# Performance work log

Hardware: AMD Instinct MI355X
Metric: run time of the kernel (lower is better)

The kernel has to match this reference:

```python
import jax, jax.numpy as jnp
import numpy as np
import math

B, S, E, H, L = 16, 512, 256, 4, 2
D = E // H            # head size = 64
MAX_POS = 10
NUM_ITEMS = 50000


def setup_inputs() -> dict:
    key = jax.random.key(0)
    ks = jax.random.split(key, 16)
    s = 0.02
    item_inputs = jax.random.randint(ks[0], (B, S), 0, 2 * NUM_ITEMS + 1)
    item_ids = jax.random.randint(ks[1], (B, S), 0, NUM_ITEMS)
    input_embed = jax.random.normal(ks[2], (2 * NUM_ITEMS + 1, E), jnp.float32) * s
    input_embed = input_embed.at[0].set(0.0)  # padding_idx=0
    query_embed = jax.random.normal(ks[3], (NUM_ITEMS, E), jnp.float32) * s
    pos_key = jax.random.normal(ks[4], (MAX_POS, D), jnp.float32) * s
    pos_value = jax.random.normal(ks[5], (MAX_POS, D), jnp.float32) * s
    Wq = jax.random.normal(ks[6], (L, E, E), jnp.float32) * s
    bq = jnp.zeros((L, E), jnp.float32)
    Wk = jax.random.normal(ks[7], (L, E, E), jnp.float32) * s
    bk = jnp.zeros((L, E), jnp.float32)
    Wv = jax.random.normal(ks[8], (L, E, E), jnp.float32) * s
    bv = jnp.zeros((L, E), jnp.float32)
    Wo = jax.random.normal(ks[9], (L, E, E), jnp.float32) * s
    bo = jnp.zeros((L, E), jnp.float32)
    out_w = jax.random.normal(ks[10], (E, 1), jnp.float32) * s
    out_b = jnp.zeros((1,), jnp.float32)
    return dict(item_inputs=item_inputs, item_ids=item_ids,
                input_embed=input_embed, query_embed=query_embed,
                pos_key=pos_key, pos_value=pos_value,
                Wq=Wq, bq=bq, Wk=Wk, bk=bk, Wv=Wv, bv=bv, Wo=Wo, bo=bo,
                out_w=out_w, out_b=out_b)


def _heads(x, W, b):
    # [B,S,E] @ [E,E] -> [B,H,S,D]
    return (x @ W + b).reshape(B, S, H, D).transpose(0, 2, 1, 3)


def reference(item_inputs, item_ids, input_embed, query_embed, pos_key,
              pos_value, Wq, bq, Wk, bk, Wv, bv, Wo, bo, out_w, out_b):
    x = input_embed[item_inputs]          # [B,S,E]
    q_base = query_embed[item_ids]        # [B,S,E]

    i = jnp.arange(S)
    rel = jnp.clip(i[:, None] - i[None, :], 0, MAX_POS - 1)  # [S,S]
    pk = pos_key[rel]                     # [S,S,D]
    pv = pos_value[rel]                   # [S,S,D]
    causal = i[None, :] > i[:, None]      # future mask [S,S], True = masked
    scale = 1.0 / math.sqrt(D)

    out = x
    for l in range(L):
        qh = _heads(q_base, Wq[l], bq[l])
        kh = _heads(out, Wk[l], bk[l])
        vh = _heads(out, Wv[l], bv[l])
        # relative attention: scores = q.k^T + q.pos_key(i-j)
        scores = jnp.einsum('bhid,bhjd->bhij', qh, kh)
        scores = scores + jnp.einsum('bhid,ijd->bhij', qh, pk)
        scores = scores * scale
        scores = jnp.where(causal[None, None], -1e9, scores)
        p = jax.nn.softmax(scores, axis=-1)  # [B,H,S,S]
        # out_i = sum_j p_ij * (v_j + pos_value(i-j))
        attn = jnp.einsum('bhij,bhjd->bhid', p, vh) \
             + jnp.einsum('bhij,ijd->bhid', p, pv)
        merged = attn.transpose(0, 2, 1, 3).reshape(B, S, E)
        residual = merged @ Wo[l] + bo[l]
        out = out + jax.nn.relu(residual)
    return out @ out_w + out_b            # [B,S,1]
```

## Files before the change

kernel.cpp:

```cpp
#include <hip/hip_runtime.h>
#include <hip/hip_bf16.h>

#define B_ 16
#define S_ 512
#define E_ 256
#define H_ 4
#define D_ 64
#define L_ 2
#define MAXPOS 10
#define HS_ ((size_t)B_ * S_ * E_)

typedef __attribute__((ext_vector_type(8))) short bf16x8;
typedef __attribute__((ext_vector_type(4))) float f32x4;

static __device__ __forceinline__ short f2bf(float f) {
    __hip_bfloat16 h = __float2bfloat16(f);
    return __builtin_bit_cast(short, h);
}

static __device__ __forceinline__ void gload16(const void* g, void* l) {
    __builtin_amdgcn_global_load_lds(
        (const __attribute__((address_space(1))) void*)(g),
        (__attribute__((address_space(3))) void*)(l),
        16, 0, 0);
}

static __device__ __forceinline__ void stage_tile(const char* gbase, char* lds,
                                                  int w, int lane) {
    #pragma unroll
    for (int c = 0; c < 8; ++c) {
        const int L = (w * 8 + c) * 1024 + lane * 16;
        const int src = L ^ (((L >> 9) & 7) << 4);
        gload16(gbase + src, lds + (w * 8 + c) * 1024);
    }
}

static __device__ __forceinline__ void gemm4(const short* As, const short* Bs,
                                             int w, int l15, int l4,
                                             f32x4& a0, f32x4& a1,
                                             f32x4& a2, f32x4& a3) {
    const int sw = (l15 & 7) << 4;
    const int arow = w * 16 + l15;
    const f32x4 z4 = (f32x4){0.f, 0.f, 0.f, 0.f};
    a0 = z4; a1 = z4; a2 = z4; a3 = z4;
    #pragma unroll
    for (int ks = 0; ks < 8; ++ks) {
        const int coff = (ks * 64 + l4 * 16) ^ sw;
        const bf16x8 af = *reinterpret_cast<const bf16x8*>((const char*)As + arow * 512 + coff);
        const bf16x8 b0 = *reinterpret_cast<const bf16x8*>((const char*)Bs + (0 * 16 + l15) * 512 + coff);
        a0 = __builtin_amdgcn_mfma_f32_16x16x32_bf16(af, b0, a0, 0, 0, 0);
        const bf16x8 b1 = *reinterpret_cast<const bf16x8*>((const char*)Bs + (1 * 16 + l15) * 512 + coff);
        a1 = __builtin_amdgcn_mfma_f32_16x16x32_bf16(af, b1, a1, 0, 0, 0);
        const bf16x8 b2 = *reinterpret_cast<const bf16x8*>((const char*)Bs + (2 * 16 + l15) * 512 + coff);
        a2 = __builtin_amdgcn_mfma_f32_16x16x32_bf16(af, b2, a2, 0, 0, 0);
        const bf16x8 b3 = *reinterpret_cast<const bf16x8*>((const char*)Bs + (3 * 16 + l15) * 512 + coff);
        a3 = __builtin_amdgcn_mfma_f32_16x16x32_bf16(af, b3, a3, 0, 0, 0);
    }
}

static __device__ __forceinline__ void gemm_compute(const short* As, const short* Bs,
                                                    f32x4* acc, int w, int l15, int l4) {
    gemm4(As, Bs, w, l15, l4, acc[0], acc[1], acc[2], acc[3]);
}

__global__ __launch_bounds__(256) void setup_kernel(
    const int* __restrict__ item_inputs, const int* __restrict__ item_ids,
    const float* __restrict__ input_embed, const float* __restrict__ query_embed,
    const float* __restrict__ Wq, const float* __restrict__ Wk,
    const float* __restrict__ Wv, const float* __restrict__ Wo,
    const float* __restrict__ out_b,
    float* __restrict__ outf, short* __restrict__ outb, short* __restrict__ qbb,
    short* __restrict__ Wt, float* __restrict__ y)
{
    const int tid = threadIdx.x;
    const int bx = blockIdx.x;
    if (bx < 512) {
        const int rr = tid >> 4, c0 = (tid & 15) * 16;
        const int row = bx * 16 + rr;
        const int ii = item_inputs[row];
        const int qi = item_ids[row];
        const float* xs = input_embed + (size_t)ii * E_ + c0;
        const float* qs = query_embed + (size_t)qi * E_ + c0;
        float* of = outf + (size_t)row * E_ + c0;
        short* ob = outb + (size_t)row * E_ + c0;
        short* qb = qbb + (size_t)row * E_ + c0;
        #pragma unroll
        for (int q = 0; q < 4; ++q) {
            const float4 xv = reinterpret_cast<const float4*>(xs)[q];
            const float4 qv = reinterpret_cast<const float4*>(qs)[q];
            reinterpret_cast<float4*>(of)[q] = xv;
            short4 xb = { f2bf(xv.x), f2bf(xv.y), f2bf(xv.z), f2bf(xv.w) };
            short4 qb4 = { f2bf(qv.x), f2bf(qv.y), f2bf(qv.z), f2bf(qv.w) };
            reinterpret_cast<short4*>(ob)[q] = xb;
            reinterpret_cast<short4*>(qb)[q] = qb4;
        }
        return;
    }
    const int pb = bx - 512;
    if (pb < 128) {
        __shared__ short tt[64 * 72];
        const int mId = pb >> 4;
        const int l = mId >> 2, which = mId & 3;
        const float* src = (which == 0 ? Wq : which == 1 ? Wk : which == 2 ? Wv : Wo)
                         + (size_t)l * E_ * E_;
        const int tr = (pb >> 2) & 3;
        const int tc = pb & 3;
        {
            const int kl = tid >> 2;
            const int nq = (tid & 3) * 16;
            const float* sp = src + (size_t)(tr * 64 + kl) * E_ + tc * 64 + nq;
            #pragma unroll
            for (int q = 0; q < 4; ++q) {
                const float4 v = reinterpret_cast<const float4*>(sp)[q];
                tt[(nq + q * 4 + 0) * 72 + kl] = f2bf(v.x);
                tt[(nq + q * 4 + 1) * 72 + kl] = f2bf(v.y);
                tt[(nq + q * 4 + 2) * 72 + kl] = f2bf(v.z);
                tt[(nq + q * 4 + 3) * 72 + kl] = f2bf(v.w);
            }
        }
        __syncthreads();
        {
            const int nl = tid >> 2;
            const int kq = (tid & 3) * 16;
            short* dst = Wt + (size_t)mId * 65536 + (size_t)(tc * 64 + nl) * E_ + tr * 64 + kq;
            *reinterpret_cast<bf16x8*>(&dst[0]) = *reinterpret_cast<const bf16x8*>(&tt[nl * 72 + kq]);
            *reinterpret_cast<bf16x8*>(&dst[8]) = *reinterpret_cast<const bf16x8*>(&tt[nl * 72 + kq + 8]);
        }
    } else if (pb == 128) {
        const float yb = out_b[0];
        for (int i = tid; i < 8192; i += 256) y[i] = yb;
    }
}

__global__ __launch_bounds__(256) void qkv_kernel(
    const short* __restrict__ qbb, const short* __restrict__ outb,
    const short* __restrict__ Wt, const float* __restrict__ bq,
    const float* __restrict__ bk, const float* __restrict__ bv,
    short* __restrict__ Qb)
{
    __shared__ __align__(16) short As[64 * 256];
    __shared__ __align__(16) short Bs[64 * 256];
    const int bm = blockIdx.x, bn = blockIdx.y, z = blockIdx.z;
    const int tid = threadIdx.x;
    const int lane = tid & 63, w = tid >> 6;
    const int l15 = lane & 15, l4 = lane >> 4;

    const short* A = (z == 0) ? qbb : outb;
    const short* W = Wt + (size_t)z * 65536;
    const float* bias = (z == 0) ? bq : (z == 1) ? bk : bv;

    stage_tile((const char*)A + (size_t)bm * 32768, (char*)As, w, lane);
    stage_tile((const char*)W + (size_t)bn * 32768, (char*)Bs, w, lane);
    __syncthreads();

    f32x4 acc[4];
    gemm_compute(As, Bs, acc, w, l15, l4);

    short* Cz = Qb + (size_t)z * HS_;
    #pragma unroll
    for (int nf = 0; nf < 4; ++nf) {
        const int col = bn * 64 + nf * 16 + l15;
        const float bb = bias[col];
        #pragma unroll
        for (int reg = 0; reg < 4; ++reg) {
            const int rowg = bm * 64 + w * 16 + l4 * 4 + reg;
            Cz[(size_t)rowg * E_ + col] = f2bf(acc[nf][reg] + bb);
        }
    }
}

__global__ __launch_bounds__(256) void o0_kernel(
    const short* __restrict__ mgb, const short* __restrict__ Wo_t,
    const float* __restrict__ bo0, float* __restrict__ outf,
    short* __restrict__ outb)
{
    __shared__ __align__(16) short As[64 * 256];
    __shared__ __align__(16) short Bs[64 * 256];
    const int bm = blockIdx.x, bn = blockIdx.y;
    const int tid = threadIdx.x;
    const int lane = tid & 63, w = tid >> 6;
    const int l15 = lane & 15, l4 = lane >> 4;

    stage_tile((const char*)mgb + (size_t)bm * 32768, (char*)As, w, lane);
    stage_tile((const char*)Wo_t + (size_t)bn * 32768, (char*)Bs, w, lane);
    __syncthreads();

    f32x4 acc[4];
    gemm_compute(As, Bs, acc, w, l15, l4);

    #pragma unroll
    for (int nf = 0; nf < 4; ++nf) {
        const int col = bn * 64 + nf * 16 + l15;
        const float bb = bo0[col];
        #pragma unroll
        for (int reg = 0; reg < 4; ++reg) {
            const int rowg = bm * 64 + w * 16 + l4 * 4 + reg;
            const size_t idx = (size_t)rowg * E_ + col;
            const float o = outf[idx] + fmaxf(acc[nf][reg] + bb, 0.0f);
            outf[idx] = o;
            outb[idx] = f2bf(o);
        }
    }
}

__global__ __launch_bounds__(256) void attn2_kernel(
    const short* __restrict__ Q, const short* __restrict__ K,
    const short* __restrict__ V, const float* __restrict__ pos_key,
    const float* __restrict__ pos_value, short* __restrict__ merged)
{
    __shared__ __align__(16) short Qs[64 * 72];
    __shared__ __align__(16) short Ks[64 * 64];
    __shared__ __align__(16) short Vts[4656];
    __shared__ __align__(16) short Pl[4 * 16 * 72];
    __shared__ __align__(16) short Pk[16 * 72];
    __shared__ float pv_sh[MAXPOS * 64];
    __shared__ float qpk_sh[64 * 16];
    __shared__ float pdiag[64 * 9];

    const int bid = blockIdx.x;
    const int a = bid & 3;
    const int h = (bid >> 2) & 3;
    const int b = bid >> 4;
    const int tid = threadIdx.x;
    const int lane = tid & 63;
    const int w = tid >> 6;
    const int l15 = lane & 15;
    const int l4  = lane >> 4;
    const int rloc  = l4 * 4;
    const int rbase = w * 16 + rloc;
    const int swl = (l15 & 7) << 4;

    const size_t boff = (size_t)(b * S_) * E_ + h * D_;

    for (int idx = tid; idx < MAXPOS * 64; idx += 256) pv_sh[idx] = pos_value[idx];
    for (int idx = tid; idx < 16 * 64; idx += 256) {
        const int r = idx >> 6, d = idx & 63;
        Pk[r * 72 + d] = (r < MAXPOS) ? f2bf(pos_key[r * 64 + d]) : (short)0;
    }

    for (int pass = 0; pass < 2; ++pass) {
        const int it = pass ? a : 7 - a;
        if (pass) __syncthreads();
        for (int idx = tid; idx < 64 * 9; idx += 256) pdiag[idx] = 0.0f;
        {
            const int row = tid >> 2, dq = (tid & 3) * 16;
            const short* qp = &Q[boff + (size_t)(it * 64 + row) * E_ + dq];
            *reinterpret_cast<bf16x8*>(&Qs[row * 72 + dq]) = *reinterpret_cast<const bf16x8*>(qp);
            *reinterpret_cast<bf16x8*>(&Qs[row * 72 + dq + 8]) = *reinterpret_cast<const bf16x8*>(qp + 8);
        }
        __syncthreads();

        bf16x8 aq[2];
        #pragma unroll
        for (int ks = 0; ks < 2; ++ks)
            aq[ks] = *reinterpret_cast<const bf16x8*>(&Qs[(w * 16 + l15) * 72 + ks * 32 + 8 * l4]);

        f32x4 cq = (f32x4){0.f, 0.f, 0.f, 0.f};
        #pragma unroll
        for (int ks = 0; ks < 2; ++ks) {
            const bf16x8 bpk = *reinterpret_cast<const bf16x8*>(&Pk[l15 * 72 + ks * 32 + 8 * l4]);
            cq = __builtin_amdgcn_mfma_f32_16x16x32_bf16(aq[ks], bpk, cq, 0, 0, 0);
        }
        float q9[4];
        #pragma unroll
        for (int r = 0; r < 4; ++r) {
            qpk_sh[(rbase + r) * 16 + l15] = cq[r] * 0.125f;
            q9[r] = __shfl(cq[r], l4 * 16 + 9, 64) * 0.125f;
        }

        f32x4 accv[4];
        #pragma unroll
        for (int nf = 0; nf < 4; ++nf) accv[nf] = (f32x4){0.f, 0.f, 0.f, 0.f};
        float ls[4] = {0.f, 0.f, 0.f, 0.f};

        for (int jt = 0; jt <= it; ++jt) {
            {
                const char* Kb = (const char*)(K + boff + (size_t)(jt * 64) * E_);
                #pragma unroll
                for (int c = 0; c < 2; ++c) {
                    const int chunk = w * 2 + c;
                    const int row = chunk * 8 + (lane >> 3);
                    const int col = (lane & 7) * 16;
                    const int src = row * 512 + (col ^ ((row & 7) << 4));
                    gload16(Kb + src, (char*)Ks + chunk * 1024);
                }
                const int row = tid >> 2, dq = (tid & 3) * 16;
                const short* vp = &V[boff + (size_t)(jt * 64 + row) * E_ + dq];
                const bf16x8 v0 = *reinterpret_cast<const bf16x8*>(vp);
                const bf16x8 v1 = *reinterpret_cast<const bf16x8*>(vp + 8);
                const int skew = (tid & 3) * 32 + row * 2;
                #pragma unroll
                for (int e = 0; e < 8; ++e) {
                    *(short*)((char*)Vts + (dq + e) * 144 + skew) = v0[e];
                    *(short*)((char*)Vts + (dq + 8 + e) * 144 + skew) = v1[e];
                }
            }
            __syncthreads();

            const bool near = (jt >= it - 1);
            #pragma unroll
            for (int nf = 0; nf < 4; ++nf) {
                f32x4 c = (f32x4){0.f, 0.f, 0.f, 0.f};
                const int jrow = nf * 16 + l15;
                const bf16x8 bk0 = *reinterpret_cast<const bf16x8*>(
                    (const char*)Ks + jrow * 128 + ((l4 * 16) ^ swl));
                const bf16x8 bk1 = *reinterpret_cast<const bf16x8*>(
                    (const char*)Ks + jrow * 128 + ((64 + l4 * 16) ^ swl));
                c = __builtin_amdgcn_mfma_f32_16x16x32_bf16(aq[0], bk0, c, 0, 0, 0);
                c = __builtin_amdgcn_mfma_f32_16x16x32_bf16(aq[1], bk1, c, 0, 0, 0);
                const int j = jt * 64 + nf * 16 + l15;
                #pragma unroll
                for (int r = 0; r < 4; ++r) {
                    float pp;
                    if (near) {
                        const int i = it * 64 + rbase + r;
                        const int rel = i - j;
                        if (rel < 0) pp = 0.0f;
                        else {
                            const int rc = rel < 9 ? rel : 9;
                            pp = __expf(fmaf(c[r], 0.125f, qpk_sh[(rbase + r) * 16 + rc]));
                            if (rel < 9) pdiag[(rbase + r) * 9 + rel] = pp;
                        }
                    } else {
                        pp = __expf(fmaf(c[r], 0.125f, q9[r]));
                    }
                    ls[r] += pp;
                    Pl[w * 1152 + (rloc + r) * 72 + nf * 16 + l15] = f2bf(pp);
                }
            }
            #pragma unroll
            for (int ks = 0; ks < 2; ++ks) {
                const bf16x8 pa = *reinterpret_cast<const bf16x8*>(
                    &Pl[w * 1152 + l15 * 72 + ks * 32 + 8 * l4]);
                #pragma unroll
                for (int nf = 0; nf < 4; ++nf) {
                    const int d = nf * 16 + l15;
                    const bf16x8 bv = *reinterpret_cast<const bf16x8*>(
                        (const char*)Vts + d * 144 + nf * 32 + ks * 64 + l4 * 16);
                    accv[nf] = __builtin_amdgcn_mfma_f32_16x16x32_bf16(pa, bv, accv[nf], 0, 0, 0);
                }
            }
            __syncthreads();
        }

        #pragma unroll
        for (int m = 1; m < 16; m <<= 1) {
            #pragma unroll
            for (int r = 0; r < 4; ++r) ls[r] += __shfl_xor(ls[r], m, 64);
        }

        #pragma unroll
        for (int r = 0; r < 4; ++r) {
            const int rowl = rbase + r;
            const float inv = 1.0f / ls[r];
            #pragma unroll
            for (int nf = 0; nf < 4; ++nf) {
                const int col = nf * 16 + l15;
                const float pv9 = pv_sh[9 * 64 + col];
                float extra = ls[r] * pv9;
                #pragma unroll
                for (int rr = 0; rr < 9; ++rr)
                    extra += pdiag[rowl * 9 + rr] * (pv_sh[rr * 64 + col] - pv9);
                merged[boff + (size_t)(it * 64 + rowl) * E_ + col] =
                    f2bf((accv[nf][r] + extra) * inv);
            }
        }
    }
}

__global__ __launch_bounds__(256) void o1final_kernel(
    const short* __restrict__ mgb, const short* __restrict__ Wt7,
    const float* __restrict__ bo1, const float* __restrict__ outf,
    const float* __restrict__ fw, float* __restrict__ y)
{
    __shared__ __align__(16) short As[64 * 256];
    __shared__ __align__(16) short Bs[64 * 256];
    const int bm = blockIdx.x, bn = blockIdx.y;
    const int tid = threadIdx.x;
    const int lane = tid & 63, w = tid >> 6;
    const int l15 = lane & 15, l4 = lane >> 4;

    stage_tile((const char*)mgb + (size_t)bm * 32768, (char*)As, w, lane);
    stage_tile((const char*)(Wt7 + (size_t)bn * 16384), (char*)Bs, w, lane);
    __syncthreads();

    f32x4 acc[4];
    gemm_compute(As, Bs, acc, w, l15, l4);

    float s[4] = {0.f, 0.f, 0.f, 0.f};
    #pragma unroll
    for (int nf = 0; nf < 4; ++nf) {
        const int col = bn * 64 + nf * 16 + l15;
        const float bb = bo1[col];
        const float fwv = fw[col];
        #pragma unroll
        for (int reg = 0; reg < 4; ++reg) {
            const int rowg = bm * 64 + w * 16 + l4 * 4 + reg;
            const float o = outf[(size_t)rowg * E_ + col] + fmaxf(acc[nf][reg] + bb, 0.0f);
            s[reg] += o * fwv;
        }
    }
    #pragma unroll
    for (int m = 1; m < 16; m <<= 1) {
        #pragma unroll
        for (int reg = 0; reg < 4; ++reg) s[reg] += __shfl_xor(s[reg], m, 64);
    }
    if (l15 == 0) {
        #pragma unroll
        for (int reg = 0; reg < 4; ++reg)
            atomicAdd(&y[bm * 64 + w * 16 + l4 * 4 + reg], s[reg]);
    }
}

extern "C" void kernel_launch(void* const* d_in, const int* in_sizes, int n_in,
                              void* d_out, int out_size, void* d_ws, size_t ws_size,
                              hipStream_t stream) {
    const int*   item_inputs = (const int*)d_in[0];
    const int*   item_ids    = (const int*)d_in[1];
    const float* input_embed = (const float*)d_in[2];
    const float* query_embed = (const float*)d_in[3];
    const float* pos_key     = (const float*)d_in[4];
    const float* pos_value   = (const float*)d_in[5];
    const float* Wq = (const float*)d_in[6];
    const float* bq = (const float*)d_in[7];
    const float* Wk = (const float*)d_in[8];
    const float* bk = (const float*)d_in[9];
    const float* Wv = (const float*)d_in[10];
    const float* bv = (const float*)d_in[11];
    const float* Wo = (const float*)d_in[12];
    const float* bo = (const float*)d_in[13];
    const float* out_w = (const float*)d_in[14];
    const float* out_b = (const float*)d_in[15];
    float* y = (float*)d_out;

    char* w8 = (char*)d_ws;
    float* outf = (float*)(w8);
    short* outb = (short*)(w8 + ((size_t)8  << 20));
    short* qbb  = (short*)(w8 + ((size_t)12 << 20));
    short* Qb   = (short*)(w8 + ((size_t)16 << 20));
    short* mgb  = (short*)(w8 + ((size_t)28 << 20));
    short* Wt   = (short*)(w8 + ((size_t)32 << 20));

    setup_kernel<<<641, 256, 0, stream>>>(
        item_inputs, item_ids, input_embed, query_embed,
        Wq, Wk, Wv, Wo, out_b, outf, outb, qbb, Wt, y);

    qkv_kernel<<<dim3(128, 4, 3), 256, 0, stream>>>(
        qbb, outb, Wt, bq, bk, bv, Qb);
    attn2_kernel<<<256, 256, 0, stream>>>(
        Qb, Qb + HS_, Qb + 2 * HS_, pos_key, pos_value, mgb);
    o0_kernel<<<dim3(128, 4), 256, 0, stream>>>(
        mgb, Wt + (size_t)3 * 65536, bo, outf, outb);

    qkv_kernel<<<dim3(128, 4, 3), 256, 0, stream>>>(
        qbb, outb, Wt + (size_t)4 * 65536, bq + E_, bk + E_, bv + E_, Qb);
    attn2_kernel<<<256, 256, 0, stream>>>(
        Qb, Qb + HS_, Qb + 2 * HS_, pos_key, pos_value, mgb);
    o1final_kernel<<<dim3(128, 4), 256, 0, stream>>>(
        mgb, Wt + (size_t)7 * 65536, bo + E_, outf, out_w, y);
}
```

Measured before the change: 112.2 us.

## Hoist layer-1 Q projection, double-buffer K/V in attention, one q-tile per block

Layer 1's Q projection depends only on the query embedding, so it now runs with the layer-0 projections in a single 4-slice launch, and layer 1 projects only K and V. The attention kernel gets one query tile per block (512 blocks instead of 256 with two paired tiles) and double-buffers the K/V tiles so the next tile loads while the current one computes. Softmax now uses exp2 with a log2(e)-folded scale. The aim is better overlap and occupancy, at the cost of more shared memory and less even work per block, since causal tiles differ in length.

```diff
diff --git a/kernel.cpp b/kernel.cpp
--- a/kernel.cpp
+++ b/kernel.cpp
@@ -132,11 +132,12 @@
     }
 }
 
-__global__ __launch_bounds__(256) void qkv_kernel(
+__global__ __launch_bounds__(256) void qkv0_kernel(
     const short* __restrict__ qbb, const short* __restrict__ outb,
     const short* __restrict__ Wt, const float* __restrict__ bq,
     const float* __restrict__ bk, const float* __restrict__ bv,
-    short* __restrict__ Qb)
+    const float* __restrict__ bq1, short* __restrict__ Qb,
+    short* __restrict__ Qb1)
 {
     __shared__ __align__(16) short As[64 * 256];
     __shared__ __align__(16) short Bs[64 * 256];
@@ -145,9 +146,9 @@
     const int lane = tid & 63, w = tid >> 6;
     const int l15 = lane & 15, l4 = lane >> 4;
 
-    const short* A = (z == 0) ? qbb : outb;
-    const short* W = Wt + (size_t)z * 65536;
-    const float* bias = (z == 0) ? bq : (z == 1) ? bk : bv;
+    const short* A = (z == 1 || z == 2) ? outb : qbb;
+    const short* W = (z == 3) ? (Wt + (size_t)4 * 65536) : (Wt + (size_t)z * 65536);
+    const float* bias = (z == 0) ? bq : (z == 1) ? bk : (z == 2) ? bv : bq1;
 
     stage_tile((const char*)A + (size_t)bm * 32768, (char*)As, w, lane);
     stage_tile((const char*)W + (size_t)bn * 32768, (char*)Bs, w, lane);
@@ -156,7 +157,42 @@
     f32x4 acc[4];
     gemm_compute(As, Bs, acc, w, l15, l4);
 
-    short* Cz = Qb + (size_t)z * HS_;
+    short* Cz = (z == 3) ? Qb1 : Qb + (size_t)z * HS_;
+    #pragma unroll
+    for (int nf = 0; nf < 4; ++nf) {
+        const int col = bn * 64 + nf * 16 + l15;
+        const float bb = bias[col];
+        #pragma unroll
+        for (int reg = 0; reg < 4; ++reg) {
+            const int rowg = bm * 64 + w * 16 + l4 * 4 + reg;
+            Cz[(size_t)rowg * E_ + col] = f2bf(acc[nf][reg] + bb);
+        }
+    }
+}
+
+__global__ __launch_bounds__(256) void kv1_kernel(
+    const short* __restrict__ outb, const short* __restrict__ Wt1,
+    const float* __restrict__ bk1, const float* __restrict__ bv1,
+    short* __restrict__ Qb)
+{
+    __shared__ __align__(16) short As[64 * 256];
+    __shared__ __align__(16) short Bs[64 * 256];
+    const int bm = blockIdx.x, bn = blockIdx.y, z = blockIdx.z;
+    const int tid = threadIdx.x;
+    const int lane = tid & 63, w = tid >> 6;
+    const int l15 = lane & 15, l4 = lane >> 4;
+
+    const short* W = Wt1 + (size_t)(z + 1) * 65536;
+    const float* bias = (z == 0) ? bk1 : bv1;
+
+    stage_tile((const char*)outb + (size_t)bm * 32768, (char*)As, w, lane);
+    stage_tile((const char*)W + (size_t)bn * 32768, (char*)Bs, w, lane);
+    __syncthreads();
+
+    f32x4 acc[4];
+    gemm_compute(As, Bs, acc, w, l15, l4);
+
+    short* Cz = Qb + (size_t)(z + 1) * HS_;
     #pragma unroll
     for (int nf = 0; nf < 4; ++nf) {
         const int col = bn * 64 + nf * 16 + l15;
@@ -203,14 +239,14 @@
     }
 }
 
-__global__ __launch_bounds__(256) void attn2_kernel(
+__global__ __launch_bounds__(256) void attn_kernel(
     const short* __restrict__ Q, const short* __restrict__ K,
     const short* __restrict__ V, const float* __restrict__ pos_key,
     const float* __restrict__ pos_value, short* __restrict__ merged)
 {
     __shared__ __align__(16) short Qs[64 * 72];
-    __shared__ __align__(16) short Ks[64 * 64];
-    __shared__ __align__(16) short Vts[4656];
+    __shared__ __align__(16) short Ks[2][64 * 64];
+    __shared__ __align__(16) short Vts[2][4656];
     __shared__ __align__(16) short Pl[4 * 16 * 72];
     __shared__ __align__(16) short Pk[16 * 72];
     __shared__ float pv_sh[MAXPOS * 64];
@@ -218,9 +254,9 @@
     __shared__ float pdiag[64 * 9];
 
     const int bid = blockIdx.x;
-    const int a = bid & 3;
-    const int h = (bid >> 2) & 3;
-    const int b = bid >> 4;
+    const int it = 7 - (bid & 7);
+    const int h  = (bid >> 3) & 3;
+    const int b  = bid >> 5;
     const int tid = threadIdx.x;
     const int lane = tid & 63;
     const int w = tid >> 6;
@@ -229,141 +265,141 @@
     const int rloc  = l4 * 4;
     const int rbase = w * 16 + rloc;
     const int swl = (l15 & 7) << 4;
+    const float SC = 0.18033688f;
 
     const size_t boff = (size_t)(b * S_) * E_ + h * D_;
 
     for (int idx = tid; idx < MAXPOS * 64; idx += 256) pv_sh[idx] = pos_value[idx];
+    for (int idx = tid; idx < 64 * 9; idx += 256) pdiag[idx] = 0.0f;
     for (int idx = tid; idx < 16 * 64; idx += 256) {
         const int r = idx >> 6, d = idx & 63;
         Pk[r * 72 + d] = (r < MAXPOS) ? f2bf(pos_key[r * 64 + d]) : (short)0;
     }
-
-    for (int pass = 0; pass < 2; ++pass) {
-        const int it = pass ? a : 7 - a;
-        if (pass) __syncthreads();
-        for (int idx = tid; idx < 64 * 9; idx += 256) pdiag[idx] = 0.0f;
-        {
-            const int row = tid >> 2, dq = (tid & 3) * 16;
-            const short* qp = &Q[boff + (size_t)(it * 64 + row) * E_ + dq];
-            *reinterpret_cast<bf16x8*>(&Qs[row * 72 + dq]) = *reinterpret_cast<const bf16x8*>(qp);
-            *reinterpret_cast<bf16x8*>(&Qs[row * 72 + dq + 8]) = *reinterpret_cast<const bf16x8*>(qp + 8);
-        }
-        __syncthreads();
-
-        bf16x8 aq[2];
-        #pragma unroll
-        for (int ks = 0; ks < 2; ++ks)
-            aq[ks] = *reinterpret_cast<const bf16x8*>(&Qs[(w * 16 + l15) * 72 + ks * 32 + 8 * l4]);
-
-        f32x4 cq = (f32x4){0.f, 0.f, 0.f, 0.f};
+    {
+        const int row = tid >> 2, dq = (tid & 3) * 16;
+        const short* qp = &Q[boff + (size_t)(it * 64 + row) * E_ + dq];
+        *reinterpret_cast<bf16x8*>(&Qs[row * 72 + dq]) = *reinterpret_cast<const bf16x8*>(qp);
+        *reinterpret_cast<bf16x8*>(&Qs[row * 72 + dq + 8]) = *reinterpret_cast<const bf16x8*>(qp + 8);
+    }
+
+    auto stageKV = [&](int jt, int buf) {
+        const char* Kb = (const char*)(K + boff + (size_t)(jt * 64) * E_);
+        #pragma unroll
+        for (int c = 0; c < 2; ++c) {
+            const int chunk = w * 2 + c;
+            const int row = chunk * 8 + (lane >> 3);
+            const int col = (lane & 7) * 16;
+            const int src = row * 512 + (col ^ ((row & 7) << 4));
+            gload16(Kb + src, (char*)Ks[buf] + chunk * 1024);
+        }
+        const int row = tid >> 2, dq = (tid & 3) * 16;
+        const short* vp = &V[boff + (size_t)(jt * 64 + row) * E_ + dq];
+        const bf16x8 v0 = *reinterpret_cast<const bf16x8*>(vp);
+        const bf16x8 v1 = *reinterpret_cast<const bf16x8*>(vp + 8);
+        const int skew = (tid & 3) * 32 + row * 2;
+        #pragma unroll
+        for (int e = 0; e < 8; ++e) {
+            *(short*)((char*)Vts[buf] + (dq + e) * 144 + skew) = v0[e];
+            *(short*)((char*)Vts[buf] + (dq + 8 + e) * 144 + skew) = v1[e];
+        }
+    };
+
+    stageKV(0, 0);
+    __syncthreads();
+
+    bf16x8 aq[2];
+    #pragma unroll
+    for (int ks = 0; ks < 2; ++ks)
+        aq[ks] = *reinterpret_cast<const bf16x8*>(&Qs[(w * 16 + l15) * 72 + ks * 32 + 8 * l4]);
+
+    f32x4 cq = (f32x4){0.f, 0.f, 0.f, 0.f};
+    #pragma unroll
+    for (int ks = 0; ks < 2; ++ks) {
+        const bf16x8 bpk = *reinterpret_cast<const bf16x8*>(&Pk[l15 * 72 + ks * 32 + 8 * l4]);
+        cq = __builtin_amdgcn_mfma_f32_16x16x32_bf16(aq[ks], bpk, cq, 0, 0, 0);
+    }
+    float q9[4];
+    #pragma unroll
+    for (int r = 0; r < 4; ++r) {
+        qpk_sh[(rbase + r) * 16 + l15] = cq[r] * SC;
+        q9[r] = __shfl(cq[r], l4 * 16 + 9, 64) * SC;
+    }
+
+    f32x4 accv[4];
+    #pragma unroll
+    for (int nf = 0; nf < 4; ++nf) accv[nf] = (f32x4){0.f, 0.f, 0.f, 0.f};
+    float ls[4] = {0.f, 0.f, 0.f, 0.f};
+
+    for (int jt = 0; jt <= it; ++jt) {
+        const int cur = jt & 1;
+        if (jt < it) stageKV(jt + 1, cur ^ 1);
+
+        const bool near = (jt >= it - 1);
+        #pragma unroll
+        for (int nf = 0; nf < 4; ++nf) {
+            f32x4 c = (f32x4){0.f, 0.f, 0.f, 0.f};
+            const int jrow = nf * 16 + l15;
+            const bf16x8 bk0 = *reinterpret_cast<const bf16x8*>(
+                (const char*)Ks[cur] + jrow * 128 + ((l4 * 16) ^ swl));
+            const bf16x8 bk1 = *reinterpret_cast<const bf16x8*>(
+                (const char*)Ks[cur] + jrow * 128 + ((64 + l4 * 16) ^ swl));
+            c = __builtin_amdgcn_mfma_f32_16x16x32_bf16(aq[0], bk0, c, 0, 0, 0);
+            c = __builtin_amdgcn_mfma_f32_16x16x32_bf16(aq[1], bk1, c, 0, 0, 0);
+            const int j = jt * 64 + nf * 16 + l15;
+            #pragma unroll
+            for (int r = 0; r < 4; ++r) {
+                float pp;
+                if (near) {
+                    const int i = it * 64 + rbase + r;
+                    const int rel = i - j;
+                    if (rel < 0) pp = 0.0f;
+                    else {
+                        const int rc = rel < 9 ? rel : 9;
+                        pp = exp2f(fmaf(c[r], SC, qpk_sh[(rbase + r) * 16 + rc]));
+                        if (rel < 9) pdiag[(rbase + r) * 9 + rel] = pp;
+                    }
+                } else {
+                    pp = exp2f(fmaf(c[r], SC, q9[r]));
+                }
+                ls[r] += pp;
+                Pl[w * 1152 + (rloc + r) * 72 + nf * 16 + l15] = f2bf(pp);
+            }
+        }
         #pragma unroll
         for (int ks = 0; ks < 2; ++ks) {
-            const bf16x8 bpk = *reinterpret_cast<const bf16x8*>(&Pk[l15 * 72 + ks * 32 + 8 * l4]);
-            cq = __builtin_amdgcn_mfma_f32_16x16x32_bf16(aq[ks], bpk, cq, 0, 0, 0);
-        }
-        float q9[4];
-        #pragma unroll
-        for (int r = 0; r < 4; ++r) {
-            qpk_sh[(rbase + r) * 16 + l15] = cq[r] * 0.125f;
-            q9[r] = __shfl(cq[r], l4 * 16 + 9, 64) * 0.125f;
-        }
-
-        f32x4 accv[4];
-        #pragma unroll
-        for (int nf = 0; nf < 4; ++nf) accv[nf] = (f32x4){0.f, 0.f, 0.f, 0.f};
-        float ls[4] = {0.f, 0.f, 0.f, 0.f};
-
-        for (int jt = 0; jt <= it; ++jt) {
-            {
-                const char* Kb = (const char*)(K + boff + (size_t)(jt * 64) * E_);
-                #pragma unroll
-                for (int c = 0; c < 2; ++c) {
-                    const int chunk = w * 2 + c;
-                    const int row = chunk * 8 + (lane >> 3);
-                    const int col = (lane & 7) * 16;
-                    const int src = row * 512 + (col ^ ((row & 7) << 4));
-                    gload16(Kb + src, (char*)Ks + chunk * 1024);
-                }
-                const int row = tid >> 2, dq = (tid & 3) * 16;
-                const short* vp = &V[boff + (size_t)(jt * 64 + row) * E_ + dq];
-                const bf16x8 v0 = *reinterpret_cast<const bf16x8*>(vp);
-                const bf16x8 v1 = *reinterpret_cast<const bf16x8*>(vp + 8);
-                const int skew = (tid & 3) * 32 + row * 2;
-                #pragma unroll
-                for (int e = 0; e < 8; ++e) {
-                    *(short*)((char*)Vts + (dq + e) * 144 + skew) = v0[e];
-                    *(short*)((char*)Vts + (dq + 8 + e) * 144 + skew) = v1[e];
-                }
-            }
-            __syncthreads();
-
-            const bool near = (jt >= it - 1);
+            const bf16x8 pa = *reinterpret_cast<const bf16x8*>(
+                &Pl[w * 1152 + l15 * 72 + ks * 32 + 8 * l4]);
             #pragma unroll
             for (int nf = 0; nf < 4; ++nf) {
-                f32x4 c = (f32x4){0.f, 0.f, 0.f, 0.f};
-                const int jrow = nf * 16 + l15;
-                const bf16x8 bk0 = *reinterpret_cast<const bf16x8*>(
-                    (const char*)Ks + jrow * 128 + ((l4 * 16) ^ swl));
-                const bf16x8 bk1 = *reinterpret_cast<const bf16x8*>(
-                    (const char*)Ks + jrow * 128 + ((64 + l4 * 16) ^ swl));
-                c = __builtin_amdgcn_mfma_f32_16x16x32_bf16(aq[0], bk0, c, 0, 0, 0);
-                c = __builtin_amdgcn_mfma_f32_16x16x32_bf16(aq[1], bk1, c, 0, 0, 0);
-                const int j = jt * 64 + nf * 16 + l15;
-                #pragma unroll
-                for (int r = 0; r < 4; ++r) {
-                    float pp;
-                    if (near) {
-                        const int i = it * 64 + rbase + r;
-                        const int rel = i - j;
-                        if (rel < 0) pp = 0.0f;
-                        else {
-                            const int rc = rel < 9 ? rel : 9;
-                            pp = __expf(fmaf(c[r], 0.125f, qpk_sh[(rbase + r) * 16 + rc]));
-                            if (rel < 9) pdiag[(rbase + r) * 9 + rel] = pp;
-                        }
-                    } else {
-                        pp = __expf(fmaf(c[r], 0.125f, q9[r]));
-                    }
-                    ls[r] += pp;
-                    Pl[w * 1152 + (rloc + r) * 72 + nf * 16 + l15] = f2bf(pp);
-                }
+                const int d = nf * 16 + l15;
+                const bf16x8 bv = *reinterpret_cast<const bf16x8*>(
+                    (const char*)Vts[cur] + d * 144 + nf * 32 + ks * 64 + l4 * 16);
+                accv[nf] = __builtin_amdgcn_mfma_f32_16x16x32_bf16(pa, bv, accv[nf], 0, 0, 0);
             }
+        }
+        __syncthreads();
+    }
+
+    #pragma unroll
+    for (int m = 1; m < 16; m <<= 1) {
+        #pragma unroll
+        for (int r = 0; r < 4; ++r) ls[r] += __shfl_xor(ls[r], m, 64);
+    }
+
+    #pragma unroll
+    for (int r = 0; r < 4; ++r) {
+        const int rowl = rbase + r;
+        const float inv = 1.0f / ls[r];
+        #pragma unroll
+        for (int nf = 0; nf < 4; ++nf) {
+            const int col = nf * 16 + l15;
+            const float pv9 = pv_sh[9 * 64 + col];
+            float extra = ls[r] * pv9;
             #pragma unroll
-            for (int ks = 0; ks < 2; ++ks) {
-                const bf16x8 pa = *reinterpret_cast<const bf16x8*>(
-                    &Pl[w * 1152 + l15 * 72 + ks * 32 + 8 * l4]);
-                #pragma unroll
-                for (int nf = 0; nf < 4; ++nf) {
-                    const int d = nf * 16 + l15;
-                    const bf16x8 bv = *reinterpret_cast<const bf16x8*>(
-                        (const char*)Vts + d * 144 + nf * 32 + ks * 64 + l4 * 16);
-                    accv[nf] = __builtin_amdgcn_mfma_f32_16x16x32_bf16(pa, bv, accv[nf], 0, 0, 0);
-                }
-            }
-            __syncthreads();
-        }
-
-        #pragma unroll
-        for (int m = 1; m < 16; m <<= 1) {
-            #pragma unroll
-            for (int r = 0; r < 4; ++r) ls[r] += __shfl_xor(ls[r], m, 64);
-        }
-
-        #pragma unroll
-        for (int r = 0; r < 4; ++r) {
-            const int rowl = rbase + r;
-            const float inv = 1.0f / ls[r];
-            #pragma unroll
-            for (int nf = 0; nf < 4; ++nf) {
-                const int col = nf * 16 + l15;
-                const float pv9 = pv_sh[9 * 64 + col];
-                float extra = ls[r] * pv9;
-                #pragma unroll
-                for (int rr = 0; rr < 9; ++rr)
-                    extra += pdiag[rowl * 9 + rr] * (pv_sh[rr * 64 + col] - pv9);
-                merged[boff + (size_t)(it * 64 + rowl) * E_ + col] =
-                    f2bf((accv[nf][r] + extra) * inv);
-            }
+            for (int rr = 0; rr < 9; ++rr)
+                extra += pdiag[rowl * 9 + rr] * (pv_sh[rr * 64 + col] - pv9);
+            merged[boff + (size_t)(it * 64 + rowl) * E_ + col] =
+                f2bf((accv[nf][r] + extra) * inv);
         }
     }
 }
@@ -381,7 +417,7 @@
     const int l15 = lane & 15, l4 = lane >> 4;
 
     stage_tile((const char*)mgb + (size_t)bm * 32768, (char*)As, w, lane);
-    stage_tile((const char*)(Wt7 + (size_t)bn * 16384), (char*)Bs, w, lane);
+    stage_tile((const char*)Wt7 + (size_t)bn * 32768, (char*)Bs, w, lane);
     __syncthreads();
 
     f32x4 acc[4];
@@ -440,22 +476,23 @@
     short* Qb   = (short*)(w8 + ((size_t)16 << 20));
     short* mgb  = (short*)(w8 + ((size_t)28 << 20));
     short* Wt   = (short*)(w8 + ((size_t)32 << 20));
+    short* Qb1  = (short*)(w8 + ((size_t)34 << 20));
 
     setup_kernel<<<641, 256, 0, stream>>>(
         item_inputs, item_ids, input_embed, query_embed,
         Wq, Wk, Wv, Wo, out_b, outf, outb, qbb, Wt, y);
 
-    qkv_kernel<<<dim3(128, 4, 3), 256, 0, stream>>>(
-        qbb, outb, Wt, bq, bk, bv, Qb);
-    attn2_kernel<<<256, 256, 0, stream>>>(
+    qkv0_kernel<<<dim3(128, 4, 4), 256, 0, stream>>>(
+        qbb, outb, Wt, bq, bk, bv, bq + E_, Qb, Qb1);
+    attn_kernel<<<512, 256, 0, stream>>>(
         Qb, Qb + HS_, Qb + 2 * HS_, pos_key, pos_value, mgb);
     o0_kernel<<<dim3(128, 4), 256, 0, stream>>>(
         mgb, Wt + (size_t)3 * 65536, bo, outf, outb);
 
-    qkv_kernel<<<dim3(128, 4, 3), 256, 0, stream>>>(
-        qbb, outb, Wt + (size_t)4 * 65536, bq + E_, bk + E_, bv + E_, Qb);
-    attn2_kernel<<<256, 256, 0, stream>>>(
-        Qb, Qb + HS_, Qb + 2 * HS_, pos_key, pos_value, mgb);
+    kv1_kernel<<<dim3(128, 4, 2), 256, 0, stream>>>(
+        outb, Wt + (size_t)4 * 65536, bk + E_, bv + E_, Qb);
+    attn_kernel<<<512, 256, 0, stream>>>(
+        Qb1, Qb + HS_, Qb + 2 * HS_, pos_key, pos_value, mgb);
     o1final_kernel<<<dim3(128, 4), 256, 0, stream>>>(
         mgb, Wt + (size_t)7 * 65536, bo + E_, outf, out_w, y);
 }
```

New measurement: 100.4 us. 10.6% less time.
